# Optimization experiments

Measured on AMD Instinct MI355X. Metric: run time of the kernel, lower is better.

The kernel has to match this reference:

```python
import jax, jax.numpy as jnp
import numpy as np
from math import sqrt

N_HEADS = 16

def _rope(t, freqs):
    # t: [b, n, l, hd]; freqs: [l, hd//2, 2] (real, imag of unit rotations)
    b, n, l, hd = t.shape
    t2 = t.reshape(b, n, l, hd // 2, 2)
    tr, ti = t2[..., 0], t2[..., 1]
    fr, fi = freqs[..., 0], freqs[..., 1]  # broadcast over b, n
    out_r = tr * fr - ti * fi
    out_i = tr * fi + ti * fr
    return jnp.stack([out_r, out_i], axis=-1).reshape(b, n, l, hd)

def setup_inputs() -> dict:
    key = jax.random.key(0)
    ks = jax.random.split(key, 6)
    B, L, D = 2, 2048, 1024
    HD = D // N_HEADS
    x = jax.random.normal(ks[0], (B, L, D), dtype=jnp.float32)
    # proper rotary frequencies: theta_i = 10000^{-2i/hd}, angle = pos * theta
    inv = 1.0 / (10000.0 ** (np.arange(0, HD, 2, dtype=np.float32) / HD))  # [HD//2]
    ang = np.arange(L, dtype=np.float32)[:, None] * inv[None, :]           # [L, HD//2]
    freqs = jnp.asarray(np.stack([np.cos(ang), np.sin(ang)], axis=-1))     # [L, HD//2, 2]
    # additive causal mask
    causal = jnp.tril(jnp.ones((L, L), dtype=bool))
    attention_mask = jnp.where(causal, 0.0, -1e9).astype(jnp.float32)[None, None]
    init = 1.0 / sqrt(D)
    Wq = jax.random.normal(ks[1], (D, D), dtype=jnp.float32) * init
    Wk = jax.random.normal(ks[2], (D, D), dtype=jnp.float32) * init
    Wv = jax.random.normal(ks[3], (D, D), dtype=jnp.float32) * init
    Wo = jax.random.normal(ks[4], (D, D), dtype=jnp.float32) * init
    return {"x": x, "freqs": freqs, "attention_mask": attention_mask,
            "Wq": Wq, "Wk": Wk, "Wv": Wv, "Wo": Wo}

def reference(x, freqs, attention_mask, Wq, Wk, Wv, Wo):
    b, l, d = x.shape
    n = N_HEADS
    hd = d // n
    scale = sqrt(hd)

    def split_heads(t):  # [b, l, d] -> [b, n, l, hd]
        return t.reshape(b, l, n, hd).transpose(0, 2, 1, 3)

    q = split_heads(x @ Wq.T)
    k = split_heads(x @ Wk.T)
    v = split_heads(x @ Wv.T)
    q = _rope(q, freqs)
    k = _rope(k, freqs)
    scores = jnp.einsum('bnqd,bnkd->bnqk', q, k) / scale
    attn = jax.nn.softmax(scores + attention_mask, axis=-1)
    out = jnp.einsum('bnqk,bnkd->bnqd', attn, v)
    out = out.transpose(0, 2, 1, 3).reshape(b, l, d)
    return out @ Wo.T
```

## Files before the change

### kernel.cpp

```cpp
#include <hip/hip_runtime.h>
#include <stdint.h>

#define LSEQ 2048
#define DMODEL 1024
#define NHEADS 16
#define HDIM 64
#define MROWS 4096

typedef __attribute__((ext_vector_type(8))) short short8;
typedef __attribute__((ext_vector_type(4))) float f32x4;
typedef __attribute__((ext_vector_type(16))) float f32x16;

static __device__ __forceinline__ unsigned short f2bf(float f) {
    unsigned u = __builtin_bit_cast(unsigned, f);
    u += 0x7fffu + ((u >> 16) & 1u);
    return (unsigned short)(u >> 16);
}
static __device__ __forceinline__ unsigned cvt_pk_bf16(float a, float b) {
    unsigned r;
    asm("v_cvt_pk_bf16_f32 %0, %1, %2" : "=v"(r) : "v"(a), "v"(b));
    return r;
}

static __device__ __forceinline__ void gl2lds16(const unsigned short* g, unsigned short* l) {
    __builtin_amdgcn_global_load_lds(
        (const __attribute__((address_space(1))) unsigned int*)g,
        (__attribute__((address_space(3))) unsigned int*)l, 16, 0, 0);
}

__global__ void cast_all(const float* __restrict__ x,  const float* __restrict__ Wq,
                         const float* __restrict__ Wk, const float* __restrict__ Wv,
                         const float* __restrict__ Wo,
                         unsigned short* __restrict__ xb,
                         unsigned short* __restrict__ wqkv,
                         unsigned short* __restrict__ wo) {
    int i = blockIdx.x * blockDim.x + threadIdx.x;
    const float4* src;
    ushort4* dst;
    if (i < 1048576) {
        src = (const float4*)x + i;
        dst = (ushort4*)xb + i;
    } else {
        int t = i - 1048576;
        int w = t >> 18;
        int j = t & 262143;
        const float* s = (w == 0) ? Wq : (w == 1) ? Wk : (w == 2) ? Wv : Wo;
        src = (const float4*)s + j;
        dst = (w == 3) ? ((ushort4*)wo + j) : ((ushort4*)wqkv + (size_t)w * 262144 + j);
    }
    float4 v = *src;
    ushort4 o;
    o.x = f2bf(v.x); o.y = f2bf(v.y); o.z = f2bf(v.z); o.w = f2bf(v.w);
    *dst = o;
}

template <int TM, bool OUT_BF16>
__global__ __launch_bounds__(256) void gemm_nt(const unsigned short* __restrict__ A,
                                               const unsigned short* __restrict__ Bw,
                                               void* __restrict__ C,
                                               int Kdim, int ldc) {
    constexpr int WM = TM / 2;
    __shared__ unsigned short As[TM * 32];
    __shared__ unsigned short Bs[128 * 32];
    int tid = threadIdx.x;
    int lane = tid & 63, wave = tid >> 6;
    int row16 = lane & 15, quad = lane >> 4;
    int wm = wave & 1, wn = wave >> 1;
    int m0 = blockIdx.x * TM;
    int n0 = blockIdx.y * 128;

    int srow = wave * 16 + (lane >> 2);
    int scol = (lane & 3) * 8;
    const unsigned short* Ag = A  + (size_t)(m0 + srow) * Kdim + scol;
    const unsigned short* Bg = Bw + (size_t)(n0 + srow) * Kdim + scol;
    unsigned short* Asw = As + wave * 512;
    unsigned short* Bsw = Bs + wave * 512;

    f32x4 acc[WM / 16][4];
    #pragma unroll
    for (int i = 0; i < WM / 16; ++i)
        #pragma unroll
        for (int j = 0; j < 4; ++j) acc[i][j] = (f32x4){0.f, 0.f, 0.f, 0.f};

    for (int k0 = 0; k0 < Kdim; k0 += 32) {
        #pragma unroll
        for (int i = 0; i < TM / 64; ++i)
            gl2lds16(Ag + (size_t)i * 64 * Kdim + k0, Asw + i * 2048);
        gl2lds16(Bg + k0, Bsw);
        gl2lds16(Bg + (size_t)64 * Kdim + k0, Bsw + 2048);
        __syncthreads();

        short8 af[WM / 16], bf_[4];
        #pragma unroll
        for (int mi = 0; mi < WM / 16; ++mi)
            af[mi] = *(const short8*)(As + (wm * WM + mi * 16 + row16) * 32 + quad * 8);
        #pragma unroll
        for (int ni = 0; ni < 4; ++ni)
            bf_[ni] = *(const short8*)(Bs + (wn * 64 + ni * 16 + row16) * 32 + quad * 8);
        #pragma unroll
        for (int mi = 0; mi < WM / 16; ++mi)
            #pragma unroll
            for (int ni = 0; ni < 4; ++ni)
                acc[mi][ni] = __builtin_amdgcn_mfma_f32_16x16x32_bf16(af[mi], bf_[ni], acc[mi][ni], 0, 0, 0);
        __syncthreads();
    }

    int orow = m0 + wm * WM + quad * 4;
    int ocol = n0 + wn * 64 + row16;
    #pragma unroll
    for (int mi = 0; mi < WM / 16; ++mi)
        #pragma unroll
        for (int ni = 0; ni < 4; ++ni)
            #pragma unroll
            for (int r = 0; r < 4; ++r) {
                size_t idx = (size_t)(orow + mi * 16 + r) * ldc + (ocol + ni * 16);
                if (OUT_BF16) ((unsigned short*)C)[idx] = f2bf(acc[mi][ni][r]);
                else          ((float*)C)[idx]          = acc[mi][ni][r];
            }
}


#define VM_NOP
#define VM_W4 asm volatile("s_waitcnt vmcnt(4)" ::: "memory");
#define VM_W0 asm volatile("s_waitcnt vmcnt(0)" ::: "memory");

#define QKV_PH(S, T, DO_STAGE, DO_AHEAD, VMW)                                 \
  {                                                                           \
    if (DO_STAGE) {                                                           \
      int ws = (((T) + 1) & 1) * 32768;                                       \
      const unsigned short* gp = ((S) & 1)                                    \
          ? (BgL + ((size_t)((T) + 1)) * 64 + ((S) >> 1) * 32)                \
          : (AgL + ((size_t)((T) + 1)) * 64 + ((S) >> 1) * 32);               \
      int ldst = ws + (((S) & 1) ? 16384 : 0) + ((S) >> 1) * 8192;            \
      gl2lds16(gp,          lds + ldst + wave * 512);                         \
      gl2lds16(gp + 131072, lds + ldst + 4096 + wave * 512);                  \
    }                                                                         \
    VMW                                                                       \
    __builtin_amdgcn_sched_barrier(0);                                        \
    __builtin_amdgcn_s_barrier();                                             \
    __builtin_amdgcn_sched_barrier(0);                                        \
    if (DO_AHEAD) {                                                           \
      const int sn = ((S) + 1) & 3;                                           \
      const int tn = ((S) == 3) ? (T) + 1 : (T);                              \
      const int rsn = (tn & 1) * 32768;                                       \
      if (sn == 0 || sn == 2) {                                               \
        const unsigned short* Bp = lds + rsn + 16384 + (sn >> 1) * 8192 + boff; \
        _Pragma("unroll")                                                     \
        for (int j = 0; j < 4; ++j)                                           \
          bfr[(sn >> 1) & 1][j] = *(const short8*)(Bp + j * 512);             \
      }                                                                       \
      const unsigned short* Ap = lds + rsn + (sn >> 1) * 8192 + aoff + (sn & 1) * 2048; \
      _Pragma("unroll")                                                       \
      for (int i = 0; i < 4; ++i)                                             \
        af[sn & 1][i] = *(const short8*)(Ap + i * 512);                       \
    }                                                                         \
    __builtin_amdgcn_sched_barrier(0);                                        \
    __builtin_amdgcn_s_setprio(1);                                            \
    _Pragma("unroll")                                                         \
    for (int i = 0; i < 4; ++i)                                               \
      _Pragma("unroll")                                                       \
      for (int j = 0; j < 4; ++j)                                             \
        acc[((S) & 1) * 4 + i][j] = __builtin_amdgcn_mfma_f32_16x16x32_bf16(  \
            af[(S) & 1][i], bfr[((S) >> 1) & 1][j], acc[((S) & 1) * 4 + i][j], 0, 0, 0); \
    __builtin_amdgcn_s_setprio(0);                                            \
    __builtin_amdgcn_s_barrier();                                             \
  }

__global__ __launch_bounds__(512, 2) void gemm_qkv(const unsigned short* __restrict__ A,
                                                   const unsigned short* __restrict__ Bw,
                                                   const float* __restrict__ freqs,
                                                   unsigned short* __restrict__ qh,
                                                   unsigned short* __restrict__ kh,
                                                   unsigned short* __restrict__ vt) {
    extern __shared__ unsigned short lds[];

    int tid  = threadIdx.x;
    int lane = tid & 63, wave = tid >> 6;
    int row16 = lane & 15, quad = lane >> 4;
    int wm = wave & 1, wn = wave >> 1;

    int id  = blockIdx.x;
    int gid = (id & 7) * 24 + (id >> 3);
    int bx = gid / 12, by = gid % 12;
    int m0 = bx * 256, n0 = by * 256;

    int off0 = tid * 16;
    int g = off0 ^ (((off0 >> 7) & 3) << 4);
    int srow = g >> 6;
    int scol = (g & 63) >> 1;
    const unsigned short* AgL = A  + (size_t)(m0 + srow) * DMODEL + scol;
    const unsigned short* BgL = Bw + (size_t)(n0 + srow) * DMODEL + scol;

    int sw   = ((row16 >> 1) & 3) << 4;
    int aoff = (wm * 128 + row16) * 32 + (((quad * 16) ^ sw) >> 1);
    int boff = (wn *  64 + row16) * 32 + (((quad * 16) ^ sw) >> 1);

    f32x4 acc[8][4];
    #pragma unroll
    for (int i = 0; i < 8; ++i)
        #pragma unroll
        for (int j = 0; j < 4; ++j) acc[i][j] = (f32x4){0.f, 0.f, 0.f, 0.f};

    gl2lds16(AgL,                lds + 0     + wave * 512);
    gl2lds16(AgL + 131072,       lds + 4096  + wave * 512);
    gl2lds16(BgL,                lds + 16384 + wave * 512);
    gl2lds16(BgL + 131072,       lds + 20480 + wave * 512);
    gl2lds16(AgL + 32,           lds + 8192  + wave * 512);
    gl2lds16(AgL + 32 + 131072,  lds + 12288 + wave * 512);
    gl2lds16(BgL + 32,           lds + 24576 + wave * 512);
    gl2lds16(BgL + 32 + 131072,  lds + 28672 + wave * 512);
    asm volatile("s_waitcnt vmcnt(4)" ::: "memory");
    __builtin_amdgcn_s_barrier();

    short8 af[2][4], bfr[2][4];
    {
        const unsigned short* Bp = lds + 16384 + boff;
        #pragma unroll
        for (int j = 0; j < 4; ++j) bfr[0][j] = *(const short8*)(Bp + j * 512);
        const unsigned short* Ap = lds + aoff;
        #pragma unroll
        for (int i = 0; i < 4; ++i) af[0][i] = *(const short8*)(Ap + i * 512);
    }

    for (int t = 0; t < 15; ++t) {
        QKV_PH(0, t, true, true, VM_NOP)
        QKV_PH(1, t, true, true, VM_W4)
        QKV_PH(2, t, true, true, VM_NOP)
        QKV_PH(3, t, true, true, VM_W4)
    }
    QKV_PH(0, 15, false, true,  VM_NOP)
    QKV_PH(1, 15, false, true,  VM_W0)
    QKV_PH(2, 15, false, true,  VM_NOP)
    QKV_PH(3, 15, false, false, VM_NOP)

    int region = n0 >> 10;
    int b = m0 >> 11;
    int orow0 = m0 + wm * 128 + quad * 4;
    int ocol0 = n0 + wn * 64 + row16;

    if (region < 2) {
        unsigned short* dst = region ? kh : qh;
        float sgn = (row16 & 1) ? 1.f : -1.f;
        #pragma unroll
        for (int nf = 0; nf < 4; ++nf) {
            int c = ocol0 - region * 1024 + nf * 16;
            int head = c >> 6, d = c & 63, ii = d >> 1;
            unsigned short* hb = dst + ((size_t)(b * NHEADS + head) * LSEQ) * HDIM + d;
            #pragma unroll
            for (int mf = 0; mf < 8; ++mf)
                #pragma unroll
                for (int r = 0; r < 4; ++r) {
                    int l = (orow0 + mf * 16 + r) & 2047;
                    float own = acc[mf][nf][r];
                    float par = __shfl_xor(own, 1);
                    float2 f = *(const float2*)(freqs + ((size_t)l * 32 + ii) * 2);
                    float out = own * f.x + par * (sgn * f.y);
                    hb[(size_t)l * HDIM] = f2bf(out);
                }
        }
    } else {
        #pragma unroll
        for (int nf = 0; nf < 4; ++nf) {
            int c = ocol0 - 2048 + nf * 16;
            int head = c >> 6, d = c & 63;
            size_t vbase = ((size_t)(b * NHEADS + head) * HDIM + d) * LSEQ;
            #pragma unroll
            for (int mf = 0; mf < 8; ++mf) {
                int l0 = (orow0 + mf * 16) & 2047;
                ushort4 o;
                o.x = f2bf(acc[mf][nf][0]);
                o.y = f2bf(acc[mf][nf][1]);
                o.z = f2bf(acc[mf][nf][2]);
                o.w = f2bf(acc[mf][nf][3]);
                *(ushort4*)(vt + vbase + l0) = o;
            }
        }
    }
}

__global__ __launch_bounds__(256, 4) void attn_flash(const unsigned short* __restrict__ qh,
                                                     const unsigned short* __restrict__ kh,
                                                     const unsigned short* __restrict__ vt,
                                                     unsigned short* __restrict__ oh) {
    __shared__ char smem[33280];
    unsigned short* ldsb = (unsigned short*)smem;
    float* mO = (float*)smem;
    float* mL = (float*)(smem + 16384);
    const float CS = 0.18033688011112042f;
    const float CB = 28.853900817779268f;

    int lane = threadIdx.x & 63;
    int wave = threadIdx.x >> 6;
    int l31 = lane & 31;
    int h   = lane >> 5;
    int kq  = wave >> 1, qq = wave & 1;

    int id  = blockIdx.x;
    int xcd = id & 7;
    int bn  = xcd * 4 + ((id >> 3) & 3);
    int p   = id >> 5;
    int b = bn >> 4, n = bn & 15;

    const unsigned short* Qb = qh + (size_t)bn * LSEQ * HDIM;
    const unsigned short* Kb = kh + (size_t)bn * LSEQ * HDIM;
    const unsigned short* Vb = vt + (size_t)bn * HDIM * LSEQ;

    int sf  = wave >> 1;
    int m0s = (wave & 1) * 2;
    const unsigned short* kg = Kb + (size_t)(sf * 32 + l31) * HDIM + m0s * 16 + h * 8;
    const unsigned short* vg = Vb + (size_t)(sf * 32 + l31) * LSEQ + m0s * 16 + h * 8;
    int soff = (sf * 4 + m0s) * 512;

    auto stage = [&](int t) {
        int sl = (t & 1) * 4096;
        const unsigned short* kgk = kg + (size_t)t * 64 * HDIM;
        const unsigned short* vgk = vg + t * 64;
        gl2lds16(kgk,      ldsb + sl + soff);
        gl2lds16(kgk + 16, ldsb + sl + soff + 512);
        gl2lds16(vgk,      ldsb + 8192 + sl + soff);
        gl2lds16(vgk + 16, ldsb + 8192 + sl + soff + 512);
    };

    auto run_qb = [&](int qb) {
        int q0 = qb * 64;
        int qabs = q0 + qq * 32 + l31;

        short8 qf[4];
        #pragma unroll
        for (int mf = 0; mf < 4; ++mf)
            qf[mf] = *(const short8*)(Qb + (size_t)(q0 + qq * 32 + l31) * HDIM + mf * 16 + h * 8);

        f32x16 accO[2];
        #pragma unroll
        for (int i = 0; i < 16; ++i) { accO[0][i] = 0.f; accO[1][i] = 0.f; }
        float l_s = 0.f;

        int nk = qb + 1;

        stage(0);
        stage(1);

        for (int kt = 0; kt < nk; ++kt) {
            if (kt < nk - 1) asm volatile("s_waitcnt vmcnt(4)" ::: "memory");
            else             asm volatile("s_waitcnt vmcnt(0)" ::: "memory");
            __builtin_amdgcn_s_barrier();
            __builtin_amdgcn_sched_barrier(0);

            int cb = (kt & 1) * 4096;
            const unsigned short* Kc = ldsb + cb;
            const unsigned short* Vc = ldsb + 8192 + cb;

            bool edge = (kt == nk - 1);
            bool dead = edge && (kq == 1) && (qq == 0);

            if (!dead) {
                f32x16 z;
                #pragma unroll
                for (int i = 0; i < 16; ++i) z[i] = 0.f;
                __builtin_amdgcn_s_setprio(1);
                #pragma unroll
                for (int m = 0; m < 4; ++m) {
                    short8 kf = *(const short8*)(Kc + (kq * 4 + m) * 512 + lane * 8);
                    z = __builtin_amdgcn_mfma_f32_32x32x16_bf16(kf, qf[m], z, 0, 0, 0);
                }
                __builtin_amdgcn_s_setprio(0);

                float p_[16];
                bool maskz = edge && (kq == qq);
                #pragma unroll
                for (int r = 0; r < 16; ++r) {
                    float e = __builtin_amdgcn_exp2f(z[r] * CS - CB);
                    if (maskz) {
                        int kabs = kt * 64 + kq * 32 + (r & 3) + 8 * (r >> 2) + 4 * h;
                        if (kabs > qabs) e = 0.f;
                    }
                    p_[r] = e;
                }
                float ps = 0.f;
                #pragma unroll
                for (int r = 0; r < 16; ++r) ps += p_[r];
                l_s += ps;

                uint2 P4[4];
                #pragma unroll
                for (int g = 0; g < 4; ++g) {
                    P4[g].x = cvt_pk_bf16(p_[4 * g],     p_[4 * g + 1]);
                    P4[g].y = cvt_pk_bf16(p_[4 * g + 2], p_[4 * g + 3]);
                }
                short8 bfr[2];
                bool hb = (h != 0);
                #pragma unroll
                for (int m = 0; m < 2; ++m) {
                    uint2 own = hb ? P4[1 + 2 * m] : P4[2 * m];
                    uint2 snd = hb ? P4[2 * m]     : P4[1 + 2 * m];
                    uint2 rcv;
                    rcv.x = __shfl_xor(snd.x, 32);
                    rcv.y = __shfl_xor(snd.y, 32);
                    uint4 bb;
                    bb.x = hb ? rcv.x : own.x;
                    bb.y = hb ? rcv.y : own.y;
                    bb.z = hb ? own.x : rcv.x;
                    bb.w = hb ? own.y : rcv.y;
                    bfr[m] = __builtin_bit_cast(short8, bb);
                }

                __builtin_amdgcn_s_setprio(1);
                #pragma unroll
                for (int dq = 0; dq < 2; ++dq)
                    #pragma unroll
                    for (int m = 0; m < 2; ++m) {
                        short8 vf = *(const short8*)(Vc + (dq * 4 + kq * 2 + m) * 512 + lane * 8);
                        accO[dq] = __builtin_amdgcn_mfma_f32_32x32x16_bf16(vf, bfr[m], accO[dq], 0, 0, 0);
                    }
                __builtin_amdgcn_s_setprio(0);
            }

            __builtin_amdgcn_sched_barrier(0);
            __builtin_amdgcn_s_barrier();
            if (kt + 2 < nk) stage(kt + 2);
        }

        l_s += __shfl_xor(l_s, 32);

        if (kq == 1) {
            #pragma unroll
            for (int dq = 0; dq < 2; ++dq)
                #pragma unroll
                for (int r = 0; r < 16; ++r)
                    mO[(qq * 2 + dq) * 1024 + r * 64 + lane] = accO[dq][r];
            mL[qq * 64 + lane] = l_s;
        }
        __syncthreads();
        if (kq == 0) {
            float inv = 1.0f / (l_s + mL[qq * 64 + lane]);
            #pragma unroll
            for (int dq = 0; dq < 2; ++dq)
                #pragma unroll
                for (int g = 0; g < 4; ++g) {
                    float o0 = (accO[dq][4 * g]     + mO[(qq * 2 + dq) * 1024 + (4 * g)     * 64 + lane]) * inv;
                    float o1 = (accO[dq][4 * g + 1] + mO[(qq * 2 + dq) * 1024 + (4 * g + 1) * 64 + lane]) * inv;
                    float o2 = (accO[dq][4 * g + 2] + mO[(qq * 2 + dq) * 1024 + (4 * g + 2) * 64 + lane]) * inv;
                    float o3 = (accO[dq][4 * g + 3] + mO[(qq * 2 + dq) * 1024 + (4 * g + 3) * 64 + lane]) * inv;
                    ushort4 o;
                    o.x = f2bf(o0); o.y = f2bf(o1); o.z = f2bf(o2); o.w = f2bf(o3);
                    int d = dq * 32 + 8 * g + 4 * h;
                    *(ushort4*)(oh + (size_t)(b * LSEQ + q0 + qq * 32 + l31) * DMODEL + n * HDIM + d) = o;
                }
        }
        __syncthreads();
    };

    run_qb(31 - p);
    run_qb(p);
}

extern "C" void kernel_launch(void* const* d_in, const int* in_sizes, int n_in,
                              void* d_out, int out_size, void* d_ws, size_t ws_size,
                              hipStream_t stream) {
    const float* x     = (const float*)d_in[0];
    const float* freqs = (const float*)d_in[1];
    const float* Wq = (const float*)d_in[3];
    const float* Wk = (const float*)d_in[4];
    const float* Wv = (const float*)d_in[5];
    const float* Wo = (const float*)d_in[6];

    char* ws = (char*)d_ws;
    unsigned short* xb   = (unsigned short*)ws; ws += (size_t)MROWS * DMODEL * 2;
    unsigned short* wqkv = (unsigned short*)ws; ws += (size_t)3 * DMODEL * DMODEL * 2;
    unsigned short* wo   = (unsigned short*)ws; ws += (size_t)DMODEL * DMODEL * 2;
    unsigned short* qh   = (unsigned short*)ws; ws += (size_t)32 * LSEQ * HDIM * 2;
    unsigned short* kh   = (unsigned short*)ws; ws += (size_t)32 * LSEQ * HDIM * 2;
    unsigned short* vt   = (unsigned short*)ws; ws += (size_t)32 * HDIM * LSEQ * 2;
    unsigned short* oh   = (unsigned short*)ws; ws += (size_t)MROWS * DMODEL * 2;

    static bool attr_set = false;
    if (!attr_set) {
        (void)hipFuncSetAttribute((const void*)gemm_qkv,
                                  hipFuncAttributeMaxDynamicSharedMemorySize, 131072);
        attr_set = true;
    }

    cast_all<<<8192, 256, 0, stream>>>(x, Wq, Wk, Wv, Wo, xb, wqkv, wo);

    gemm_qkv<<<192, 512, 131072, stream>>>(xb, wqkv, freqs, qh, kh, vt);

    attn_flash<<<512, 256, 0, stream>>>(qh, kh, vt, oh);

    gemm_nt<64, false><<<dim3(MROWS / 64, DMODEL / 128), 256, 0, stream>>>(oh, wo, (float*)d_out, DMODEL, DMODEL);
}
```

Baseline: 198.8 us.

## Replace QKV and output GEMMs with unified 128x128 double-buffered kernel

Drops the 256x256, 512-thread phase-macro QKV GEMM and the simple single-buffered output GEMM. Both are replaced by one templated 128x128-tile, 256-thread kernel that loads 64-wide K chunks into swizzled LDS with double buffering. The QKV launch goes from 192 to 768 blocks, which should fill the CUs better, at the cost of less data reuse per tile. The output projection gains prefetch pipelining and larger tiles in place of the 64x128 no-overlap loop.

```diff
diff --git a/kernel.cpp b/kernel.cpp
--- a/kernel.cpp
+++ b/kernel.cpp
@@ -54,124 +54,14 @@
     *dst = o;
 }
 
-template <int TM, bool OUT_BF16>
-__global__ __launch_bounds__(256) void gemm_nt(const unsigned short* __restrict__ A,
-                                               const unsigned short* __restrict__ Bw,
-                                               void* __restrict__ C,
-                                               int Kdim, int ldc) {
-    constexpr int WM = TM / 2;
-    __shared__ unsigned short As[TM * 32];
-    __shared__ unsigned short Bs[128 * 32];
-    int tid = threadIdx.x;
-    int lane = tid & 63, wave = tid >> 6;
-    int row16 = lane & 15, quad = lane >> 4;
-    int wm = wave & 1, wn = wave >> 1;
-    int m0 = blockIdx.x * TM;
-    int n0 = blockIdx.y * 128;
-
-    int srow = wave * 16 + (lane >> 2);
-    int scol = (lane & 3) * 8;
-    const unsigned short* Ag = A  + (size_t)(m0 + srow) * Kdim + scol;
-    const unsigned short* Bg = Bw + (size_t)(n0 + srow) * Kdim + scol;
-    unsigned short* Asw = As + wave * 512;
-    unsigned short* Bsw = Bs + wave * 512;
-
-    f32x4 acc[WM / 16][4];
-    #pragma unroll
-    for (int i = 0; i < WM / 16; ++i)
-        #pragma unroll
-        for (int j = 0; j < 4; ++j) acc[i][j] = (f32x4){0.f, 0.f, 0.f, 0.f};
-
-    for (int k0 = 0; k0 < Kdim; k0 += 32) {
-        #pragma unroll
-        for (int i = 0; i < TM / 64; ++i)
-            gl2lds16(Ag + (size_t)i * 64 * Kdim + k0, Asw + i * 2048);
-        gl2lds16(Bg + k0, Bsw);
-        gl2lds16(Bg + (size_t)64 * Kdim + k0, Bsw + 2048);
-        __syncthreads();
-
-        short8 af[WM / 16], bf_[4];
-        #pragma unroll
-        for (int mi = 0; mi < WM / 16; ++mi)
-            af[mi] = *(const short8*)(As + (wm * WM + mi * 16 + row16) * 32 + quad * 8);
-        #pragma unroll
-        for (int ni = 0; ni < 4; ++ni)
-            bf_[ni] = *(const short8*)(Bs + (wn * 64 + ni * 16 + row16) * 32 + quad * 8);
-        #pragma unroll
-        for (int mi = 0; mi < WM / 16; ++mi)
-            #pragma unroll
-            for (int ni = 0; ni < 4; ++ni)
-                acc[mi][ni] = __builtin_amdgcn_mfma_f32_16x16x32_bf16(af[mi], bf_[ni], acc[mi][ni], 0, 0, 0);
-        __syncthreads();
-    }
-
-    int orow = m0 + wm * WM + quad * 4;
-    int ocol = n0 + wn * 64 + row16;
-    #pragma unroll
-    for (int mi = 0; mi < WM / 16; ++mi)
-        #pragma unroll
-        for (int ni = 0; ni < 4; ++ni)
-            #pragma unroll
-            for (int r = 0; r < 4; ++r) {
-                size_t idx = (size_t)(orow + mi * 16 + r) * ldc + (ocol + ni * 16);
-                if (OUT_BF16) ((unsigned short*)C)[idx] = f2bf(acc[mi][ni][r]);
-                else          ((float*)C)[idx]          = acc[mi][ni][r];
-            }
-}
-
-
-#define VM_NOP
-#define VM_W4 asm volatile("s_waitcnt vmcnt(4)" ::: "memory");
-#define VM_W0 asm volatile("s_waitcnt vmcnt(0)" ::: "memory");
-
-#define QKV_PH(S, T, DO_STAGE, DO_AHEAD, VMW)                                 \
-  {                                                                           \
-    if (DO_STAGE) {                                                           \
-      int ws = (((T) + 1) & 1) * 32768;                                       \
-      const unsigned short* gp = ((S) & 1)                                    \
-          ? (BgL + ((size_t)((T) + 1)) * 64 + ((S) >> 1) * 32)                \
-          : (AgL + ((size_t)((T) + 1)) * 64 + ((S) >> 1) * 32);               \
-      int ldst = ws + (((S) & 1) ? 16384 : 0) + ((S) >> 1) * 8192;            \
-      gl2lds16(gp,          lds + ldst + wave * 512);                         \
-      gl2lds16(gp + 131072, lds + ldst + 4096 + wave * 512);                  \
-    }                                                                         \
-    VMW                                                                       \
-    __builtin_amdgcn_sched_barrier(0);                                        \
-    __builtin_amdgcn_s_barrier();                                             \
-    __builtin_amdgcn_sched_barrier(0);                                        \
-    if (DO_AHEAD) {                                                           \
-      const int sn = ((S) + 1) & 3;                                           \
-      const int tn = ((S) == 3) ? (T) + 1 : (T);                              \
-      const int rsn = (tn & 1) * 32768;                                       \
-      if (sn == 0 || sn == 2) {                                               \
-        const unsigned short* Bp = lds + rsn + 16384 + (sn >> 1) * 8192 + boff; \
-        _Pragma("unroll")                                                     \
-        for (int j = 0; j < 4; ++j)                                           \
-          bfr[(sn >> 1) & 1][j] = *(const short8*)(Bp + j * 512);             \
-      }                                                                       \
-      const unsigned short* Ap = lds + rsn + (sn >> 1) * 8192 + aoff + (sn & 1) * 2048; \
-      _Pragma("unroll")                                                       \
-      for (int i = 0; i < 4; ++i)                                             \
-        af[sn & 1][i] = *(const short8*)(Ap + i * 512);                       \
-    }                                                                         \
-    __builtin_amdgcn_sched_barrier(0);                                        \
-    __builtin_amdgcn_s_setprio(1);                                            \
-    _Pragma("unroll")                                                         \
-    for (int i = 0; i < 4; ++i)                                               \
-      _Pragma("unroll")                                                       \
-      for (int j = 0; j < 4; ++j)                                             \
-        acc[((S) & 1) * 4 + i][j] = __builtin_amdgcn_mfma_f32_16x16x32_bf16(  \
-            af[(S) & 1][i], bfr[((S) >> 1) & 1][j], acc[((S) & 1) * 4 + i][j], 0, 0, 0); \
-    __builtin_amdgcn_s_setprio(0);                                            \
-    __builtin_amdgcn_s_barrier();                                             \
-  }
-
-__global__ __launch_bounds__(512, 2) void gemm_qkv(const unsigned short* __restrict__ A,
-                                                   const unsigned short* __restrict__ Bw,
-                                                   const float* __restrict__ freqs,
-                                                   unsigned short* __restrict__ qh,
-                                                   unsigned short* __restrict__ kh,
-                                                   unsigned short* __restrict__ vt) {
+template <int MODE, int NBY>
+__global__ __launch_bounds__(256, 2) void gemm128(const unsigned short* __restrict__ A,
+                                                  const unsigned short* __restrict__ Bw,
+                                                  const float* __restrict__ freqs,
+                                                  unsigned short* __restrict__ qh,
+                                                  unsigned short* __restrict__ kh,
+                                                  unsigned short* __restrict__ vt,
+                                                  float* __restrict__ C) {
     extern __shared__ unsigned short lds[];
 
     int tid  = threadIdx.x;
@@ -180,63 +70,90 @@
     int wm = wave & 1, wn = wave >> 1;
 
     int id  = blockIdx.x;
-    int gid = (id & 7) * 24 + (id >> 3);
-    int bx = gid / 12, by = gid % 12;
-    int m0 = bx * 256, n0 = by * 256;
+    int gid = (id & 7) * (4 * NBY) + (id >> 3);
+    int bx = gid / NBY, by = gid % NBY;
+    int m0 = bx * 128, n0 = by * 128;
 
     int off0 = tid * 16;
     int g = off0 ^ (((off0 >> 7) & 3) << 4);
     int srow = g >> 6;
     int scol = (g & 63) >> 1;
-    const unsigned short* AgL = A  + (size_t)(m0 + srow) * DMODEL + scol;
-    const unsigned short* BgL = Bw + (size_t)(n0 + srow) * DMODEL + scol;
+    const unsigned short* Ag = A  + (size_t)(m0 + srow) * DMODEL + scol;
+    const unsigned short* Bg = Bw + (size_t)(n0 + srow) * DMODEL + scol;
 
     int sw   = ((row16 >> 1) & 3) << 4;
-    int aoff = (wm * 128 + row16) * 32 + (((quad * 16) ^ sw) >> 1);
-    int boff = (wn *  64 + row16) * 32 + (((quad * 16) ^ sw) >> 1);
-
-    f32x4 acc[8][4];
+    int aoff = (wm * 64 + row16) * 32 + (((quad * 16) ^ sw) >> 1);
+    int boff = (wn * 64 + row16) * 32 + (((quad * 16) ^ sw) >> 1);
+
+    f32x4 acc[4][4];
     #pragma unroll
-    for (int i = 0; i < 8; ++i)
+    for (int i = 0; i < 4; ++i)
         #pragma unroll
         for (int j = 0; j < 4; ++j) acc[i][j] = (f32x4){0.f, 0.f, 0.f, 0.f};
 
-    gl2lds16(AgL,                lds + 0     + wave * 512);
-    gl2lds16(AgL + 131072,       lds + 4096  + wave * 512);
-    gl2lds16(BgL,                lds + 16384 + wave * 512);
-    gl2lds16(BgL + 131072,       lds + 20480 + wave * 512);
-    gl2lds16(AgL + 32,           lds + 8192  + wave * 512);
-    gl2lds16(AgL + 32 + 131072,  lds + 12288 + wave * 512);
-    gl2lds16(BgL + 32,           lds + 24576 + wave * 512);
-    gl2lds16(BgL + 32 + 131072,  lds + 28672 + wave * 512);
-    asm volatile("s_waitcnt vmcnt(4)" ::: "memory");
-    __builtin_amdgcn_s_barrier();
-
-    short8 af[2][4], bfr[2][4];
-    {
-        const unsigned short* Bp = lds + 16384 + boff;
-        #pragma unroll
-        for (int j = 0; j < 4; ++j) bfr[0][j] = *(const short8*)(Bp + j * 512);
-        const unsigned short* Ap = lds + aoff;
-        #pragma unroll
-        for (int i = 0; i < 4; ++i) af[0][i] = *(const short8*)(Ap + i * 512);
+    auto stage = [&](int t) {
+        int bo = (t & 1) * 16384;
+        const unsigned short* As_ = Ag + t * 64;
+        const unsigned short* Bs_ = Bg + t * 64;
+        gl2lds16(As_,                 lds + bo + 0     + wave * 512);
+        gl2lds16(As_ + 64 * DMODEL,   lds + bo + 2048  + wave * 512);
+        gl2lds16(As_ + 32,            lds + bo + 4096  + wave * 512);
+        gl2lds16(As_ + 32 + 64 * DMODEL, lds + bo + 6144 + wave * 512);
+        gl2lds16(Bs_,                 lds + bo + 8192  + wave * 512);
+        gl2lds16(Bs_ + 64 * DMODEL,   lds + bo + 10240 + wave * 512);
+        gl2lds16(Bs_ + 32,            lds + bo + 12288 + wave * 512);
+        gl2lds16(Bs_ + 32 + 64 * DMODEL, lds + bo + 14336 + wave * 512);
+    };
+
+    stage(0);
+    stage(1);
+
+    for (int t = 0; t < 16; ++t) {
+        if (t < 15) asm volatile("s_waitcnt vmcnt(8)" ::: "memory");
+        else        asm volatile("s_waitcnt vmcnt(0)" ::: "memory");
+        __builtin_amdgcn_s_barrier();
+        __builtin_amdgcn_sched_barrier(0);
+
+        int bo = (t & 1) * 16384;
+        #pragma unroll
+        for (int kk = 0; kk < 2; ++kk) {
+            short8 af[4], bfr[4];
+            const unsigned short* Ap = lds + bo + kk * 4096 + aoff;
+            const unsigned short* Bp = lds + bo + 8192 + kk * 4096 + boff;
+            #pragma unroll
+            for (int i = 0; i < 4; ++i) af[i] = *(const short8*)(Ap + i * 512);
+            #pragma unroll
+            for (int j = 0; j < 4; ++j) bfr[j] = *(const short8*)(Bp + j * 512);
+            __builtin_amdgcn_s_setprio(1);
+            #pragma unroll
+            for (int i = 0; i < 4; ++i)
+                #pragma unroll
+                for (int j = 0; j < 4; ++j)
+                    acc[i][j] = __builtin_amdgcn_mfma_f32_16x16x32_bf16(af[i], bfr[j], acc[i][j], 0, 0, 0);
+            __builtin_amdgcn_s_setprio(0);
+        }
+
+        __builtin_amdgcn_sched_barrier(0);
+        __builtin_amdgcn_s_barrier();
+        if (t + 2 < 16) stage(t + 2);
     }
 
-    for (int t = 0; t < 15; ++t) {
-        QKV_PH(0, t, true, true, VM_NOP)
-        QKV_PH(1, t, true, true, VM_W4)
-        QKV_PH(2, t, true, true, VM_NOP)
-        QKV_PH(3, t, true, true, VM_W4)
+    int orow0 = m0 + wm * 64 + quad * 4;
+    int ocol0 = n0 + wn * 64 + row16;
+
+    if (MODE == 1) {
+        #pragma unroll
+        for (int mi = 0; mi < 4; ++mi)
+            #pragma unroll
+            for (int ni = 0; ni < 4; ++ni)
+                #pragma unroll
+                for (int r = 0; r < 4; ++r)
+                    C[(size_t)(orow0 + mi * 16 + r) * DMODEL + (ocol0 + ni * 16)] = acc[mi][ni][r];
+        return;
     }
-    QKV_PH(0, 15, false, true,  VM_NOP)
-    QKV_PH(1, 15, false, true,  VM_W0)
-    QKV_PH(2, 15, false, true,  VM_NOP)
-    QKV_PH(3, 15, false, false, VM_NOP)
 
     int region = n0 >> 10;
     int b = m0 >> 11;
-    int orow0 = m0 + wm * 128 + quad * 4;
-    int ocol0 = n0 + wn * 64 + row16;
 
     if (region < 2) {
         unsigned short* dst = region ? kh : qh;
@@ -247,7 +164,7 @@
             int head = c >> 6, d = c & 63, ii = d >> 1;
             unsigned short* hb = dst + ((size_t)(b * NHEADS + head) * LSEQ) * HDIM + d;
             #pragma unroll
-            for (int mf = 0; mf < 8; ++mf)
+            for (int mf = 0; mf < 4; ++mf)
                 #pragma unroll
                 for (int r = 0; r < 4; ++r) {
                     int l = (orow0 + mf * 16 + r) & 2047;
@@ -265,7 +182,7 @@
             int head = c >> 6, d = c & 63;
             size_t vbase = ((size_t)(b * NHEADS + head) * HDIM + d) * LSEQ;
             #pragma unroll
-            for (int mf = 0; mf < 8; ++mf) {
+            for (int mf = 0; mf < 4; ++mf) {
                 int l0 = (orow0 + mf * 16) & 2047;
                 ushort4 o;
                 o.x = f2bf(acc[mf][nf][0]);
@@ -475,16 +392,18 @@
 
     static bool attr_set = false;
     if (!attr_set) {
-        (void)hipFuncSetAttribute((const void*)gemm_qkv,
-                                  hipFuncAttributeMaxDynamicSharedMemorySize, 131072);
+        (void)hipFuncSetAttribute((const void*)gemm128<0, 24>,
+                                  hipFuncAttributeMaxDynamicSharedMemorySize, 65536);
+        (void)hipFuncSetAttribute((const void*)gemm128<1, 8>,
+                                  hipFuncAttributeMaxDynamicSharedMemorySize, 65536);
         attr_set = true;
     }
 
     cast_all<<<8192, 256, 0, stream>>>(x, Wq, Wk, Wv, Wo, xb, wqkv, wo);
 
-    gemm_qkv<<<192, 512, 131072, stream>>>(xb, wqkv, freqs, qh, kh, vt);
+    gemm128<0, 24><<<768, 256, 65536, stream>>>(xb, wqkv, freqs, qh, kh, vt, nullptr);
 
     attn_flash<<<512, 256, 0, stream>>>(qh, kh, vt, oh);
 
-    gemm_nt<64, false><<<dim3(MROWS / 64, DMODEL / 128), 256, 0, stream>>>(oh, wo, (float*)d_out, DMODEL, DMODEL);
-}
+    gemm128<1, 8><<<256, 256, 65536, stream>>>(oh, wo, nullptr, nullptr, nullptr, nullptr, (float*)d_out);
+}
```

After: 186.1 us. 6.4% less time.
